# Optimization experiments

Measured on AMD Instinct MI355X. Metric: run time of the kernel, lower is better.

The kernel has to match this reference:

```python
import jax, jax.numpy as jnp
import numpy as np

HIDDEN = 4096
NUM_EXPERTS = 64
TOKENS = 16384
TOP_K = 2


def setup_inputs() -> dict:
    key = jax.random.key(0)
    kx, kw = jax.random.split(key)
    x = jax.random.normal(kx, (TOKENS, HIDDEN), dtype=jnp.float32)
    # router gate weight, as in nn.Parameter(torch.randn(num_experts, hidden_size))
    weight = jax.random.normal(kw, (NUM_EXPERTS, HIDDEN), dtype=jnp.float32)
    return {"x": x, "weight": weight}


def reference(x, weight):
    # logits = F.linear(x, weight)  -> [tokens, num_experts]
    logits = jnp.einsum("th,eh->te", x, weight)
    # top-2 experts per token, then softmax over the 2 selected logits
    top_vals, selected_experts = jax.lax.top_k(logits, TOP_K)  # [tokens, 2]
    weights = jax.nn.softmax(top_vals, axis=-1)
    return weights, selected_experts
```

## Files before the change

### kernel.cpp

```cpp
#include <hip/hip_runtime.h>
#include <math.h>

#define TOKENS 16384
#define HIDDEN 4096
#define NEXP   64
#define NSL    4
#define KSL    (HIDDEN / NSL)
#define TOKB   64
#define NCH    (KSL / 32)

typedef _Float16 half8 __attribute__((ext_vector_type(8)));
typedef float    f32x4 __attribute__((ext_vector_type(4)));

__global__ void w_prep(const float* __restrict__ W,
                       _Float16* __restrict__ Wh, _Float16* __restrict__ Wl) {
    int idx = blockIdx.x * blockDim.x + threadIdx.x;
    int e = idx >> 12;
    int k = idx & 4095;
    float v = W[idx];
    _Float16 h = (_Float16)v;
    _Float16 l = (_Float16)(v - (float)h);
    size_t dst = (((size_t)(k >> 5) * NEXP) + e) * 32 + (k & 31);
    Wh[dst] = h;
    Wl[dst] = l;
}

__global__ __launch_bounds__(256, 4) void router_mfma(
    const float* __restrict__ x, const _Float16* __restrict__ Wh,
    const _Float16* __restrict__ Wl, float* __restrict__ partial)
{
    const int tid  = threadIdx.x;
    const int lane = tid & 63;
    const int wv   = tid >> 6;
    const int e16  = lane & 15;
    const int quad = lane >> 4;

    const int tok0 = blockIdx.x * TOKB + wv * 16;
    const int sl   = blockIdx.y;
    const int kb0  = sl * (KSL / 32);

    f32x4 acc[4];
    #pragma unroll
    for (int n = 0; n < 4; ++n) acc[n] = (f32x4){0.f, 0.f, 0.f, 0.f};

    const float* xp = x + (size_t)(tok0 + e16) * HIDDEN + sl * KSL + quad * 8;

    float4 pa0 = *(const float4*)(xp);
    float4 pa1 = *(const float4*)(xp + 4);

    for (int c = 0; c < NCH; ++c) {
        float av[8] = {pa0.x, pa0.y, pa0.z, pa0.w, pa1.x, pa1.y, pa1.z, pa1.w};
        if (c + 1 < NCH) {
            pa0 = *(const float4*)(xp + (c + 1) * 32);
            pa1 = *(const float4*)(xp + (c + 1) * 32 + 4);
        }

        const size_t bo = (((size_t)(kb0 + c) * NEXP) + e16) * 32 + quad * 8;
        half8 bh[4], bl[4];
        #pragma unroll
        for (int n = 0; n < 4; ++n) {
            bh[n] = *reinterpret_cast<const half8*>(Wh + bo + (size_t)n * 16 * 32);
            bl[n] = *reinterpret_cast<const half8*>(Wl + bo + (size_t)n * 16 * 32);
        }

        half8 ah, al;
        #pragma unroll
        for (int j = 0; j < 8; ++j) {
            _Float16 h = (_Float16)av[j];
            ah[j] = h;
            al[j] = (_Float16)(av[j] - (float)h);
        }

        #pragma unroll
        for (int n = 0; n < 4; ++n)
            acc[n] = __builtin_amdgcn_mfma_f32_16x16x32_f16(al, bh[n], acc[n], 0, 0, 0);
        #pragma unroll
        for (int n = 0; n < 4; ++n)
            acc[n] = __builtin_amdgcn_mfma_f32_16x16x32_f16(ah, bl[n], acc[n], 0, 0, 0);
        #pragma unroll
        for (int n = 0; n < 4; ++n)
            acc[n] = __builtin_amdgcn_mfma_f32_16x16x32_f16(ah, bh[n], acc[n], 0, 0, 0);
    }

    #pragma unroll
    for (int n = 0; n < 4; ++n) {
        float* pb = partial + ((size_t)sl * NEXP + n * 16 + e16) * TOKENS
                  + tok0 + quad * 4;
        *reinterpret_cast<float4*>(pb) =
            make_float4(acc[n][0], acc[n][1], acc[n][2], acc[n][3]);
    }
}

__global__ void reduce_topk(const float* __restrict__ partial,
                            float* __restrict__ out)
{
    int t = blockIdx.x * blockDim.x + threadIdx.x;
    float v1 = -INFINITY, v2 = -INFINITY;
    int i1 = 0, i2 = 0;
    #pragma unroll 4
    for (int e = 0; e < NEXP; ++e) {
        float v = 0.f;
        #pragma unroll
        for (int s = 0; s < NSL; ++s)
            v += partial[((size_t)s * NEXP + e) * TOKENS + t];
        if (v > v1)      { v2 = v1; i2 = i1; v1 = v; i1 = e; }
        else if (v > v2) { v2 = v;  i2 = e; }
    }
    float e2 = expf(v2 - v1);
    float d  = 1.f / (1.f + e2);
    out[t * 2 + 0] = d;
    out[t * 2 + 1] = e2 * d;
    out[2 * TOKENS + t * 2 + 0] = (float)i1;
    out[2 * TOKENS + t * 2 + 1] = (float)i2;
}

extern "C" void kernel_launch(void* const* d_in, const int* in_sizes, int n_in,
                              void* d_out, int out_size, void* d_ws, size_t ws_size,
                              hipStream_t stream) {
    const float* x = (const float*)d_in[0];
    const float* W = (const float*)d_in[1];
    float* out = (float*)d_out;

    _Float16* Wh = (_Float16*)d_ws;
    _Float16* Wl = Wh + (size_t)NEXP * HIDDEN;
    float* partial = (float*)((char*)d_ws + 2 * (size_t)NEXP * HIDDEN * sizeof(_Float16));

    w_prep<<<(NEXP * HIDDEN) / 256, 256, 0, stream>>>(W, Wh, Wl);
    dim3 grid(TOKENS / TOKB, NSL);
    router_mfma<<<grid, 256, 0, stream>>>(x, Wh, Wl, partial);
    reduce_topk<<<TOKENS / 256, 256, 0, stream>>>(partial, out);
}
```

Measured before the change: 421.4 us.

## Process two token tiles per wave to reuse weight fragments, double K-splits

```diff
diff --git a/kernel.cpp b/kernel.cpp
--- a/kernel.cpp
+++ b/kernel.cpp
@@ -4,9 +4,9 @@
 #define TOKENS 16384
 #define HIDDEN 4096
 #define NEXP   64
-#define NSL    4
+#define NSL    8
 #define KSL    (HIDDEN / NSL)
-#define TOKB   64
+#define TOKB   128
 #define NCH    (KSL / 32)
 
 typedef _Float16 half8 __attribute__((ext_vector_type(8)));
@@ -25,6 +25,17 @@
     Wl[dst] = l;
 }
 
+__device__ __forceinline__ void split8(const float4& p0, const float4& p1,
+                                       half8& h, half8& l) {
+    const float v[8] = {p0.x, p0.y, p0.z, p0.w, p1.x, p1.y, p1.z, p1.w};
+    #pragma unroll
+    for (int j = 0; j < 8; ++j) {
+        _Float16 hi = (_Float16)v[j];
+        h[j] = hi;
+        l[j] = (_Float16)(v[j] - (float)hi);
+    }
+}
+
 __global__ __launch_bounds__(256, 4) void router_mfma(
     const float* __restrict__ x, const _Float16* __restrict__ Wh,
     const _Float16* __restrict__ Wl, float* __restrict__ partial)
@@ -35,26 +46,24 @@
     const int e16  = lane & 15;
     const int quad = lane >> 4;
 
-    const int tok0 = blockIdx.x * TOKB + wv * 16;
+    const int tok0 = blockIdx.x * TOKB + wv * 32;
     const int sl   = blockIdx.y;
-    const int kb0  = sl * (KSL / 32);
+    const int kb0  = sl * NCH;
 
-    f32x4 acc[4];
+    f32x4 accA[4], accB[4];
     #pragma unroll
-    for (int n = 0; n < 4; ++n) acc[n] = (f32x4){0.f, 0.f, 0.f, 0.f};
+    for (int n = 0; n < 4; ++n) {
+        accA[n] = (f32x4){0.f, 0.f, 0.f, 0.f};
+        accB[n] = (f32x4){0.f, 0.f, 0.f, 0.f};
+    }
 
-    const float* xp = x + (size_t)(tok0 + e16) * HIDDEN + sl * KSL + quad * 8;
+    const float* xpA = x + (size_t)(tok0 + e16) * HIDDEN + sl * KSL + quad * 8;
+    const float* xpB = xpA + (size_t)16 * HIDDEN;
 
-    float4 pa0 = *(const float4*)(xp);
-    float4 pa1 = *(const float4*)(xp + 4);
+    float4 pA0 = *(const float4*)(xpA),     pA1 = *(const float4*)(xpA + 4);
+    float4 pB0 = *(const float4*)(xpB),     pB1 = *(const float4*)(xpB + 4);
 
     for (int c = 0; c < NCH; ++c) {
-        float av[8] = {pa0.x, pa0.y, pa0.z, pa0.w, pa1.x, pa1.y, pa1.z, pa1.w};
-        if (c + 1 < NCH) {
-            pa0 = *(const float4*)(xp + (c + 1) * 32);
-            pa1 = *(const float4*)(xp + (c + 1) * 32 + 4);
-        }
-
         const size_t bo = (((size_t)(kb0 + c) * NEXP) + e16) * 32 + quad * 8;
         half8 bh[4], bl[4];
         #pragma unroll
@@ -63,23 +72,34 @@
             bl[n] = *reinterpret_cast<const half8*>(Wl + bo + (size_t)n * 16 * 32);
         }
 
-        half8 ah, al;
-        #pragma unroll
-        for (int j = 0; j < 8; ++j) {
-            _Float16 h = (_Float16)av[j];
-            ah[j] = h;
-            al[j] = (_Float16)(av[j] - (float)h);
+        half8 ahA, alA, ahB, alB;
+        split8(pA0, pA1, ahA, alA);
+        split8(pB0, pB1, ahB, alB);
+        if (c + 1 < NCH) {
+            pA0 = *(const float4*)(xpA + (c + 1) * 32);
+            pA1 = *(const float4*)(xpA + (c + 1) * 32 + 4);
+            pB0 = *(const float4*)(xpB + (c + 1) * 32);
+            pB1 = *(const float4*)(xpB + (c + 1) * 32 + 4);
         }
 
         #pragma unroll
         for (int n = 0; n < 4; ++n)
-            acc[n] = __builtin_amdgcn_mfma_f32_16x16x32_f16(al, bh[n], acc[n], 0, 0, 0);
+            accA[n] = __builtin_amdgcn_mfma_f32_16x16x32_f16(alA, bh[n], accA[n], 0, 0, 0);
         #pragma unroll
         for (int n = 0; n < 4; ++n)
-            acc[n] = __builtin_amdgcn_mfma_f32_16x16x32_f16(ah, bl[n], acc[n], 0, 0, 0);
+            accB[n] = __builtin_amdgcn_mfma_f32_16x16x32_f16(alB, bh[n], accB[n], 0, 0, 0);
         #pragma unroll
         for (int n = 0; n < 4; ++n)
-            acc[n] = __builtin_amdgcn_mfma_f32_16x16x32_f16(ah, bh[n], acc[n], 0, 0, 0);
+            accA[n] = __builtin_amdgcn_mfma_f32_16x16x32_f16(ahA, bl[n], accA[n], 0, 0, 0);
+        #pragma unroll
+        for (int n = 0; n < 4; ++n)
+            accB[n] = __builtin_amdgcn_mfma_f32_16x16x32_f16(ahB, bl[n], accB[n], 0, 0, 0);
+        #pragma unroll
+        for (int n = 0; n < 4; ++n)
+            accA[n] = __builtin_amdgcn_mfma_f32_16x16x32_f16(ahA, bh[n], accA[n], 0, 0, 0);
+        #pragma unroll
+        for (int n = 0; n < 4; ++n)
+            accB[n] = __builtin_amdgcn_mfma_f32_16x16x32_f16(ahB, bh[n], accB[n], 0, 0, 0);
     }
 
     #pragma unroll
@@ -87,7 +107,9 @@
         float* pb = partial + ((size_t)sl * NEXP + n * 16 + e16) * TOKENS
                   + tok0 + quad * 4;
         *reinterpret_cast<float4*>(pb) =
-            make_float4(acc[n][0], acc[n][1], acc[n][2], acc[n][3]);
+            make_float4(accA[n][0], accA[n][1], accA[n][2], accA[n][3]);
+        *reinterpret_cast<float4*>(pb + 16) =
+            make_float4(accB[n][0], accB[n][1], accB[n][2], accB[n][3]);
     }
 }
 
@@ -128,5 +150,5 @@
     w_prep<<<(NEXP * HIDDEN) / 256, 256, 0, stream>>>(W, Wh, Wl);
     dim3 grid(TOKENS / TOKB, NSL);
     router_mfma<<<grid, 256, 0, stream>>>(x, Wh, Wl, partial);
-    reduce_topk<<<TOKENS / 256, 256, 0, stream>>>(partial, out);
+    reduce_topk<<<TOKENS / 128, 128, 0, stream>>>(partial, out);
 }
```

New measurement: 404.4 us. 4.0% less time.

## Fuse split-K GEMM with top-2 reduction and double-buffer operand loads

Applied to the files above, without the earlier changes.

```diff
diff --git a/kernel.cpp b/kernel.cpp
--- a/kernel.cpp
+++ b/kernel.cpp
@@ -4,10 +4,9 @@
 #define TOKENS 16384
 #define HIDDEN 4096
 #define NEXP   64
-#define NSL    4
-#define KSL    (HIDDEN / NSL)
-#define TOKB   64
-#define NCH    (KSL / 32)
+#define NCH    (HIDDEN / 32)
+#define TPB    128
+#define TOKB   32
 
 typedef _Float16 half8 __attribute__((ext_vector_type(8)));
 typedef float    f32x4 __attribute__((ext_vector_type(4)));
@@ -25,10 +24,23 @@
     Wl[dst] = l;
 }
 
-__global__ __launch_bounds__(256, 4) void router_mfma(
+__device__ __forceinline__ void split8(const float4& p0, const float4& p1,
+                                       half8& h, half8& l) {
+    const float v[8] = {p0.x, p0.y, p0.z, p0.w, p1.x, p1.y, p1.z, p1.w};
+    #pragma unroll
+    for (int j = 0; j < 8; ++j) {
+        _Float16 hi = (_Float16)v[j];
+        h[j] = hi;
+        l[j] = (_Float16)(v[j] - (float)hi);
+    }
+}
+
+__global__ __launch_bounds__(TPB, 1) void router_fused(
     const float* __restrict__ x, const _Float16* __restrict__ Wh,
-    const _Float16* __restrict__ Wl, float* __restrict__ partial)
+    const _Float16* __restrict__ Wl, float* __restrict__ out)
 {
+    __shared__ float lds[2][16][NEXP + 1];
+
     const int tid  = threadIdx.x;
     const int lane = tid & 63;
     const int wv   = tid >> 6;
@@ -36,82 +48,82 @@
     const int quad = lane >> 4;
 
     const int tok0 = blockIdx.x * TOKB + wv * 16;
-    const int sl   = blockIdx.y;
-    const int kb0  = sl * (KSL / 32);
 
     f32x4 acc[4];
     #pragma unroll
     for (int n = 0; n < 4; ++n) acc[n] = (f32x4){0.f, 0.f, 0.f, 0.f};
 
-    const float* xp = x + (size_t)(tok0 + e16) * HIDDEN + sl * KSL + quad * 8;
+    const float* xp = x + (size_t)(tok0 + e16) * HIDDEN + quad * 8;
 
-    float4 pa0 = *(const float4*)(xp);
-    float4 pa1 = *(const float4*)(xp + 4);
+    float4 a0[2], a1[2];
+    a0[0] = *(const float4*)(xp);        a1[0] = *(const float4*)(xp + 4);
+    a0[1] = *(const float4*)(xp + 32);   a1[1] = *(const float4*)(xp + 36);
 
-    for (int c = 0; c < NCH; ++c) {
-        float av[8] = {pa0.x, pa0.y, pa0.z, pa0.w, pa1.x, pa1.y, pa1.z, pa1.w};
-        if (c + 1 < NCH) {
-            pa0 = *(const float4*)(xp + (c + 1) * 32);
-            pa1 = *(const float4*)(xp + (c + 1) * 32 + 4);
-        }
-
-        const size_t bo = (((size_t)(kb0 + c) * NEXP) + e16) * 32 + quad * 8;
-        half8 bh[4], bl[4];
+    half8 bh[2][4], bl[2][4];
+    {
+        const size_t bo = (size_t)e16 * 32 + quad * 8;
         #pragma unroll
         for (int n = 0; n < 4; ++n) {
-            bh[n] = *reinterpret_cast<const half8*>(Wh + bo + (size_t)n * 16 * 32);
-            bl[n] = *reinterpret_cast<const half8*>(Wl + bo + (size_t)n * 16 * 32);
+            bh[0][n] = *reinterpret_cast<const half8*>(Wh + bo + (size_t)n * 512);
+            bl[0][n] = *reinterpret_cast<const half8*>(Wl + bo + (size_t)n * 512);
         }
+    }
+
+    #pragma unroll 2
+    for (int c = 0; c < NCH; ++c) {
+        const int cur = c & 1, nxt = cur ^ 1;
 
         half8 ah, al;
-        #pragma unroll
-        for (int j = 0; j < 8; ++j) {
-            _Float16 h = (_Float16)av[j];
-            ah[j] = h;
-            al[j] = (_Float16)(av[j] - (float)h);
+        split8(a0[cur], a1[cur], ah, al);
+
+        if (c + 2 < NCH) {
+            a0[cur] = *(const float4*)(xp + (c + 2) * 32);
+            a1[cur] = *(const float4*)(xp + (c + 2) * 32 + 4);
+        }
+        if (c + 1 < NCH) {
+            const size_t bo = ((size_t)(c + 1) * NEXP + e16) * 32 + quad * 8;
+            #pragma unroll
+            for (int n = 0; n < 4; ++n) {
+                bh[nxt][n] = *reinterpret_cast<const half8*>(Wh + bo + (size_t)n * 512);
+                bl[nxt][n] = *reinterpret_cast<const half8*>(Wl + bo + (size_t)n * 512);
+            }
         }
 
         #pragma unroll
         for (int n = 0; n < 4; ++n)
-            acc[n] = __builtin_amdgcn_mfma_f32_16x16x32_f16(al, bh[n], acc[n], 0, 0, 0);
+            acc[n] = __builtin_amdgcn_mfma_f32_16x16x32_f16(al, bh[cur][n], acc[n], 0, 0, 0);
         #pragma unroll
         for (int n = 0; n < 4; ++n)
-            acc[n] = __builtin_amdgcn_mfma_f32_16x16x32_f16(ah, bl[n], acc[n], 0, 0, 0);
+            acc[n] = __builtin_amdgcn_mfma_f32_16x16x32_f16(ah, bl[cur][n], acc[n], 0, 0, 0);
         #pragma unroll
         for (int n = 0; n < 4; ++n)
-            acc[n] = __builtin_amdgcn_mfma_f32_16x16x32_f16(ah, bh[n], acc[n], 0, 0, 0);
+            acc[n] = __builtin_amdgcn_mfma_f32_16x16x32_f16(ah, bh[cur][n], acc[n], 0, 0, 0);
     }
 
     #pragma unroll
-    for (int n = 0; n < 4; ++n) {
-        float* pb = partial + ((size_t)sl * NEXP + n * 16 + e16) * TOKENS
-                  + tok0 + quad * 4;
-        *reinterpret_cast<float4*>(pb) =
-            make_float4(acc[n][0], acc[n][1], acc[n][2], acc[n][3]);
+    for (int n = 0; n < 4; ++n)
+        #pragma unroll
+        for (int r = 0; r < 4; ++r)
+            lds[wv][quad * 4 + r][n * 16 + e16] = acc[n][r];
+    __syncthreads();
+
+    if (lane < 16) {
+        float v1 = -INFINITY, v2 = -INFINITY;
+        int i1 = 0, i2 = 0;
+        #pragma unroll 8
+        for (int e = 0; e < NEXP; ++e) {
+            float v = lds[wv][lane][e];
+            if (v > v1)      { v2 = v1; i2 = i1; v1 = v; i1 = e; }
+            else if (v > v2) { v2 = v;  i2 = e; }
+        }
+        float e2 = expf(v2 - v1);
+        float d  = 1.f / (1.f + e2);
+        int tok = tok0 + lane;
+        out[tok * 2 + 0] = d;
+        out[tok * 2 + 1] = e2 * d;
+        out[2 * TOKENS + tok * 2 + 0] = (float)i1;
+        out[2 * TOKENS + tok * 2 + 1] = (float)i2;
     }
-}
-
-__global__ void reduce_topk(const float* __restrict__ partial,
-                            float* __restrict__ out)
-{
-    int t = blockIdx.x * blockDim.x + threadIdx.x;
-    float v1 = -INFINITY, v2 = -INFINITY;
-    int i1 = 0, i2 = 0;
-    #pragma unroll 4
-    for (int e = 0; e < NEXP; ++e) {
-        float v = 0.f;
-        #pragma unroll
-        for (int s = 0; s < NSL; ++s)
-            v += partial[((size_t)s * NEXP + e) * TOKENS + t];
-        if (v > v1)      { v2 = v1; i2 = i1; v1 = v; i1 = e; }
-        else if (v > v2) { v2 = v;  i2 = e; }
-    }
-    float e2 = expf(v2 - v1);
-    float d  = 1.f / (1.f + e2);
-    out[t * 2 + 0] = d;
-    out[t * 2 + 1] = e2 * d;
-    out[2 * TOKENS + t * 2 + 0] = (float)i1;
-    out[2 * TOKENS + t * 2 + 1] = (float)i2;
 }
 
 extern "C" void kernel_launch(void* const* d_in, const int* in_sizes, int n_in,
@@ -123,10 +135,7 @@
 
     _Float16* Wh = (_Float16*)d_ws;
     _Float16* Wl = Wh + (size_t)NEXP * HIDDEN;
-    float* partial = (float*)((char*)d_ws + 2 * (size_t)NEXP * HIDDEN * sizeof(_Float16));
 
     w_prep<<<(NEXP * HIDDEN) / 256, 256, 0, stream>>>(W, Wh, Wl);
-    dim3 grid(TOKENS / TOKB, NSL);
-    router_mfma<<<grid, 256, 0, stream>>>(x, Wh, Wl, partial);
-    reduce_topk<<<TOKENS / 256, 256, 0, stream>>>(partial, out);
+    router_fused<<<TOKENS / TOKB, TPB, 0, stream>>>(x, Wh, Wl, out);
 }
```

Result: faster. 408.7 us (-3.0%).
